# Kernel optimization log

Hardware: AMD Instinct MI355X
Metric: run time of the kernel (lower is better)

## Reference

```python
import jax, jax.numpy as jnp
import numpy as np

N_TAYLOR = 4

def taylor_exp_poly(x, n_terms):
    # sum_{p=0}^{n_terms-1} x^p / p!  via Horner: 1 + x*(1 + x/2*(1 + x/3*(...)))
    acc = jnp.ones_like(x)
    for p in range(n_terms - 1, 0, -1):
        acc = 1.0 + (x / p) * acc
    return acc

def setup_inputs() -> dict:
    key = jax.random.key(0)
    kq, kk, kv = jax.random.split(key, 3)
    B, H, T, d_key, d_val = 4, 8, 2048, 32, 64
    Q = jax.random.normal(kq, (B, H, T, d_key), dtype=jnp.float32)
    K = jax.random.normal(kk, (B, H, T, d_key), dtype=jnp.float32)
    V = jax.random.normal(kv, (B, H, T, d_val), dtype=jnp.float32)
    return {"Q": Q, "K": K, "V": V}

def reference(Q, K, V):
    # Symmetry-aware Taylor-approximated attention (Heinsen & Kozachkov).
    # The tightly-packed degree-p feature maps phi_p satisfy
    #   phi_p(q) . phi_p(k) == (q.k / sqrt(d_key))^p / p!
    # so summing S/Z over all n_taylor terms equals attention with kernel
    #   w(q,k) = sum_{p<n_taylor} (q.k/sqrt(d_key))^p / p!   (truncated exp),
    # causally masked and normalized by the row-sum Z.
    d_key = Q.shape[-1]
    scale = 1.0 / jnp.sqrt(jnp.asarray(d_key, dtype=Q.dtype))
    scores = jnp.einsum('bhqd,bhkd->bhqk', Q, K) * scale  # [B,H,T,T]
    A = taylor_exp_poly(scores, N_TAYLOR)
    T = Q.shape[-2]
    causal = jnp.tril(jnp.ones((T, T), dtype=bool))  # [T,T]
    A = jnp.where(causal, A, jnp.zeros((), dtype=A.dtype))
    Z = jnp.sum(A, axis=-1, keepdims=True)           # [B,H,T,1]
    S = jnp.einsum('bhqk,bhkd->bhqd', A, V)          # [B,H,T,d_val]
    return S / Z
```

## Files before the change

kernel.cpp:

```cpp
#include <hip/hip_runtime.h>
#include <hip/hip_bf16.h>


typedef __attribute__((ext_vector_type(8))) short bf16x8;
typedef __attribute__((ext_vector_type(8))) _Float16 f16x8;
typedef __attribute__((ext_vector_type(4))) float f32x4;
typedef __attribute__((ext_vector_type(16))) float f32x16;
typedef unsigned int u32;
typedef unsigned short u16;

namespace {

constexpr int T_SEQ = 2048;
constexpr int DK    = 32;
constexpr int DV    = 64;
constexpr int NBH   = 32;

constexpr float C1 = 0.17677669529663687f;
constexpr float C2 = 0.015625f;
constexpr float C3 = 9.2071195e-4f;

constexpr size_t KHF_OFF  = 0;
constexpr size_t VTHI_OFF = (size_t)NBH * T_SEQ * DK * 2;
constexpr size_t WS_NEED  = VTHI_OFF + (size_t)NBH * DV * T_SEQ * 2;

__device__ __forceinline__ u32 pack_hi2(float f0, float f1) {
  return (__float_as_uint(f0) >> 16) | (__float_as_uint(f1) & 0xffff0000u);
}
__device__ __forceinline__ float trunc_bf(float f) {
  return __uint_as_float(__float_as_uint(f) & 0xffff0000u);
}
__device__ __forceinline__ u16 f2h(float f) {
  union { _Float16 h; u16 u; } c;
  c.h = (_Float16)f;
  return c.u;
}
__device__ __forceinline__ u32 pack_rn2(float f0, float f1) {
  union { __hip_bfloat16 h; u16 u; } a, b;
  a.h = __hip_bfloat16(f0);
  b.h = __hip_bfloat16(f1);
  return (u32)a.u | ((u32)b.u << 16);
}
__device__ __forceinline__ void permswap(u32& a, u32& b) {
  asm volatile("v_permlane32_swap_b32 %0, %1" : "+v"(a), "+v"(b));
}


__global__ void pack_kv(const float* __restrict__ Kg, const float* __restrict__ Vg,
                        u16* __restrict__ Khf, u16* __restrict__ Vthi) {
  __shared__ float tile[DV][33];
  const int bid = blockIdx.x;
  const int t   = threadIdx.x;
  if (bid < 2048) {
    size_t i = ((size_t)bid * 256 + t) * 4;
    float4 f = *(const float4*)(Kg + i);
    ushort4 h;
    h.x = f2h(f.x); h.y = f2h(f.y); h.z = f2h(f.z); h.w = f2h(f.w);
    *(ushort4*)(Khf + i) = h;
  } else {
    const int vb = bid - 2048;
    const int bh = vb >> 6;
    const int k0 = (vb & 63) * 32;
    {
      const int kl = t >> 3, c0 = (t & 7) * 8;
      const float* src = Vg + ((size_t)bh * T_SEQ + k0 + kl) * DV + c0;
      float4 a = *(const float4*)src;
      float4 b = *(const float4*)(src + 4);
      tile[c0 + 0][kl] = a.x; tile[c0 + 1][kl] = a.y;
      tile[c0 + 2][kl] = a.z; tile[c0 + 3][kl] = a.w;
      tile[c0 + 4][kl] = b.x; tile[c0 + 5][kl] = b.y;
      tile[c0 + 6][kl] = b.z; tile[c0 + 7][kl] = b.w;
    }
    __syncthreads();
    {
      const int cl = t >> 2, k8 = (t & 3) * 8;
      u32 h[4];
#pragma unroll
      for (int j = 0; j < 4; ++j)
        h[j] = pack_rn2(tile[cl][k8 + 2 * j], tile[cl][k8 + 2 * j + 1]);
      size_t off = ((size_t)(bh * DV + cl)) * T_SEQ + k0 + k8;
      *(uint4*)(Vthi + off) = make_uint4(h[0], h[1], h[2], h[3]);
    }
  }
}


__global__ __launch_bounds__(256, 4)
void taylor_attn_v7(const float* __restrict__ Qg, const u16* __restrict__ Khf,
                    const u16* __restrict__ Vthi, float* __restrict__ Outg) {
  __shared__ __align__(16) float Sp[4 * 2048];
  __shared__ float Zp[4 * 32];

  const int tid = threadIdx.x;
  const int l   = tid & 63;
  const int w   = tid >> 6;
  const int cq  = l & 31;
  const int hi  = l >> 5;

  const int bid = blockIdx.x;
  const int xcd = bid & 7;
  const int r_  = bid >> 3;
  const int bh  = xcd * 4 + (r_ & 3);
  const int p   = r_ >> 2;

  const u16* kq = Khf + (size_t)bh * T_SEQ * DK + (size_t)cq * DK + hi * 8;
  const u16* vq = Vthi + (size_t)bh * DV * T_SEQ + (size_t)cq * T_SEQ + hi * 8;
  const float* qb = Qg + (size_t)bh * T_SEQ * DK;

#pragma unroll 1
  for (int ph = 0; ph < 2; ++ph) {
    const int s  = ph ? (63 - p) : p;
    const int q0 = s * 32;

    if (ph) __syncthreads();

    f16x8 qf[2];
#pragma unroll
    for (int t = 0; t < 2; ++t) {
      const float* qp = qb + (size_t)(q0 + cq) * DK + t * 16 + hi * 8;
      float4 a = *(const float4*)qp;
      float4 b = *(const float4*)(qp + 4);
      f16x8 v;
      v[0] = (_Float16)a.x; v[1] = (_Float16)a.y;
      v[2] = (_Float16)a.z; v[3] = (_Float16)a.w;
      v[4] = (_Float16)b.x; v[5] = (_Float16)b.y;
      v[6] = (_Float16)b.z; v[7] = (_Float16)b.w;
      qf[t] = v;
    }

    f32x16 acc0, acc1;
#pragma unroll
    for (int r = 0; r < 16; ++r) { acc0[r] = 0.f; acc1[r] = 0.f; }
    float zacc = 0.f;

    auto LOADK = [&](f16x8* kf, int kt) {
      const u16* kp = kq + (size_t)kt * 1024;
      kf[0] = *(const f16x8*)kp;
      kf[1] = *(const f16x8*)(kp + 16);
    };
    auto LOADV = [&](bf16x8* vf, int kt) {
#pragma unroll
      for (int ct = 0; ct < 2; ++ct)
#pragma unroll
        for (int t = 0; t < 2; ++t)
          vf[ct * 2 + t] = *(const bf16x8*)(
              vq + (size_t)ct * 32 * T_SEQ + kt * 32 + t * 16);
    };
    auto STEP = [&](const f16x8* kf, const bf16x8* vf, bool diag) {
      f32x16 d;
#pragma unroll
      for (int r = 0; r < 16; ++r) d[r] = 0.f;
      d = __builtin_amdgcn_mfma_f32_32x32x16_f16(kf[0], qf[0], d, 0, 0, 0);
      d = __builtin_amdgcn_mfma_f32_32x32x16_f16(kf[1], qf[1], d, 0, 0, 0);
      float wv[16];
#pragma unroll
      for (int r = 0; r < 16; ++r) {
        float sc = d[r];
        float t_ = __builtin_fmaf(sc, C3, C2);
        t_       = __builtin_fmaf(sc, t_, C1);
        float wr = __builtin_fmaf(sc, t_, 1.0f);
        if (diag) {
          const int krel = (r & 3) + 8 * (r >> 2) + 4 * hi;
          wr = (krel <= cq) ? wr : 0.f;
        }
        zacc += wr;
        wv[r] = wr;
      }
      union { bf16x8 v; u32 u[4]; } WH[2];
#pragma unroll
      for (int t = 0; t < 2; ++t) {
        const int b = t * 8;
        u32 p0 = pack_rn2(wv[b + 0], wv[b + 1]);
        u32 p1 = pack_rn2(wv[b + 2], wv[b + 3]);
        u32 p2 = pack_rn2(wv[b + 4], wv[b + 5]);
        u32 p3 = pack_rn2(wv[b + 6], wv[b + 7]);
        permswap(p0, p2); permswap(p1, p3);
        WH[t].u[0] = p0; WH[t].u[1] = p1; WH[t].u[2] = p2; WH[t].u[3] = p3;
      }
      acc0 = __builtin_amdgcn_mfma_f32_32x32x16_bf16(WH[0].v, vf[0], acc0, 0, 0, 0);
      acc0 = __builtin_amdgcn_mfma_f32_32x32x16_bf16(WH[1].v, vf[1], acc0, 0, 0, 0);
      acc1 = __builtin_amdgcn_mfma_f32_32x32x16_bf16(WH[0].v, vf[2], acc1, 0, 0, 0);
      acc1 = __builtin_amdgcn_mfma_f32_32x32x16_bf16(WH[1].v, vf[3], acc1, 0, 0, 0);
    };

    int kt = w;
    f16x8 kA[2], kB[2];
    if (kt < s) {
      LOADK(kA, kt);
      while (true) {
        int kn = kt + 4;
        if (kn < s) {
          LOADK(kB, kn);
          bf16x8 vf[4]; LOADV(vf, kt);
          STEP(kA, vf, false);
          kt = kn;
        } else {
          bf16x8 vf[4]; LOADV(vf, kt);
          STEP(kA, vf, false);
          break;
        }
        kn = kt + 4;
        if (kn < s) {
          LOADK(kA, kn);
          bf16x8 vf[4]; LOADV(vf, kt);
          STEP(kB, vf, false);
          kt = kn;
        } else {
          bf16x8 vf[4]; LOADV(vf, kt);
          STEP(kB, vf, false);
          break;
        }
      }
    }
    if ((s & 3) == w) {
      f16x8 kD[2]; LOADK(kD, s);
      bf16x8 vf[4]; LOADV(vf, s);
      STEP(kD, vf, true);
    }

    {
      float zt = zacc + __shfl_xor(zacc, 32);
      if (hi == 0) Zp[w * 32 + cq] = zt;
    }
#pragma unroll
    for (int r = 0; r < 16; ++r) {
      const int qr = (r & 3) + 8 * (r >> 2) + 4 * hi;
      Sp[w * 2048 + qr * 64 + cq]      = acc0[r];
      Sp[w * 2048 + qr * 64 + 32 + cq] = acc1[r];
    }
    __syncthreads();

    const f32x4* S4 = (const f32x4*)Sp;
#pragma unroll
    for (int i = 0; i < 2; ++i) {
      const int e4  = tid + i * 256;
      const int row = e4 >> 4;
      f32x4 ssum = S4[e4] + S4[512 + e4] + S4[1024 + e4] + S4[1536 + e4];
      float z = Zp[row] + Zp[32 + row] + Zp[64 + row] + Zp[96 + row];
      float inv = 1.0f / z;
      float4 o;
      o.x = ssum[0] * inv; o.y = ssum[1] * inv;
      o.z = ssum[2] * inv; o.w = ssum[3] * inv;
      *(float4*)(Outg + ((size_t)bh * T_SEQ + q0 + row) * DV + (e4 & 15) * 4) = o;
    }
  }
}


constexpr int QT_FB = 64;
constexpr int KT_FB = 32;
constexpr int LDSW  = 40;
constexpr float SCALE = 0.17677669529663687f;

__global__ __launch_bounds__(256, 4)
void taylor_attn_fb(const float* __restrict__ Qg, const float* __restrict__ Kg,
                    const float* __restrict__ Vg, float* __restrict__ Outg) {
  __shared__ __align__(16) unsigned short Qhi[QT_FB * LDSW], Qlo[QT_FB * LDSW];
  __shared__ __align__(16) unsigned short Khi_[KT_FB * LDSW], Klo_[KT_FB * LDSW];
  __shared__ __align__(16) unsigned short Vthi_[DV * LDSW], Vtlo_[DV * LDSW];
  __shared__ __align__(16) unsigned Wp[4][16 * 32];

  const int tid  = threadIdx.x;
  const int lane = tid & 63;
  const int wid  = tid >> 6;
  const int m    = lane & 15;
  const int g    = lane >> 4;

  const int bid = blockIdx.x;
  const int v   = bid >> 3;
  const int bh  = (bid & 7) * 4 + (v >> 5);
  const int qt  = 31 - (v & 31);
  const int q0  = qt * QT_FB;

  const float* Qbase = Qg + ((size_t)bh * T_SEQ + q0) * DK;
  const float* Kbase = Kg + (size_t)bh * T_SEQ * DK;
  const float* Vbase = Vg + (size_t)bh * T_SEQ * DV;

#pragma unroll
  for (int p = 0; p < 2; ++p) {
    int e = tid + p * 256, row = e >> 3, c4 = (e & 7) * 4;
    float4 f = *(const float4*)(Qbase + row * DK + c4);
    uint2 h, l;
    h.x = pack_hi2(f.x, f.y); h.y = pack_hi2(f.z, f.w);
    l.x = pack_hi2(f.x - trunc_bf(f.x), f.y - trunc_bf(f.y));
    l.y = pack_hi2(f.z - trunc_bf(f.z), f.w - trunc_bf(f.w));
    *(uint2*)&Qhi[row * LDSW + c4] = h;
    *(uint2*)&Qlo[row * LDSW + c4] = l;
  }
  __syncthreads();

  const int wq = wid * 16;
  const bf16x8 qhi = *(const bf16x8*)&Qhi[(wq + m) * LDSW + g * 8];
  const bf16x8 qlo = *(const bf16x8*)&Qlo[(wq + m) * LDSW + g * 8];

  f32x4 acc[4];
#pragma unroll
  for (int ct = 0; ct < 4; ++ct) acc[ct] = f32x4{0.f, 0.f, 0.f, 0.f};
  float zacc[4] = {0.f, 0.f, 0.f, 0.f};

  const int q_lane0 = q0 + wq + g * 4;
  const int q_wave_max = q0 + wq + 15;

  const int nkt = (q0 + QT_FB) / KT_FB;
  for (int kt = 0; kt < nkt; ++kt) {
    const int k0 = kt * KT_FB;
    __syncthreads();
    {
      int row = tid >> 3, c4 = (tid & 7) * 4;
      float4 f = *(const float4*)(Kbase + (size_t)(k0 + row) * DK + c4);
      uint2 h, l;
      h.x = pack_hi2(f.x, f.y); h.y = pack_hi2(f.z, f.w);
      l.x = pack_hi2(f.x - trunc_bf(f.x), f.y - trunc_bf(f.y));
      l.y = pack_hi2(f.z - trunc_bf(f.z), f.w - trunc_bf(f.w));
      *(uint2*)&Khi_[row * LDSW + c4] = h;
      *(uint2*)&Klo_[row * LDSW + c4] = l;
    }
    {
      int kk = (tid & 15) * 2, c4 = (tid >> 4) * 4;
      const float* vp = Vbase + (size_t)(k0 + kk) * DV + c4;
      float4 a = *(const float4*)vp;
      float4 b = *(const float4*)(vp + DV);
      float af[4] = {a.x, a.y, a.z, a.w};
      float bf_[4] = {b.x, b.y, b.z, b.w};
#pragma unroll
      for (int jj = 0; jj < 4; ++jj) {
        *(unsigned*)&Vthi_[(c4 + jj) * LDSW + kk] = pack_hi2(af[jj], bf_[jj]);
        *(unsigned*)&Vtlo_[(c4 + jj) * LDSW + kk] =
            pack_hi2(af[jj] - trunc_bf(af[jj]), bf_[jj] - trunc_bf(bf_[jj]));
      }
    }
    __syncthreads();

    if (k0 > q_wave_max) continue;

#pragma unroll
    for (int k16 = 0; k16 < 2; ++k16) {
      const int kcol0 = k16 * 16;
      bf16x8 khi = *(const bf16x8*)&Khi_[(kcol0 + m) * LDSW + g * 8];
      bf16x8 klo = *(const bf16x8*)&Klo_[(kcol0 + m) * LDSW + g * 8];
      f32x4 sc = {0.f, 0.f, 0.f, 0.f};
      sc = __builtin_amdgcn_mfma_f32_16x16x32_bf16(qhi, khi, sc, 0, 0, 0);
      sc = __builtin_amdgcn_mfma_f32_16x16x32_bf16(qhi, klo, sc, 0, 0, 0);
      sc = __builtin_amdgcn_mfma_f32_16x16x32_bf16(qlo, khi, sc, 0, 0, 0);
      const int k_abs = k0 + kcol0 + m;
      const int kcol  = kcol0 + m;
#pragma unroll
      for (int r = 0; r < 4; ++r) {
        float x  = sc[r] * SCALE;
        float a3 = __builtin_fmaf(x, 0.3333333333333333f, 1.0f);
        float a2 = __builtin_fmaf(x * 0.5f, a3, 1.0f);
        float wvv = __builtin_fmaf(x, a2, 1.0f);
        wvv = (k_abs <= q_lane0 + r) ? wvv : 0.0f;
        zacc[r] += wvv;
        float wl = wvv - trunc_bf(wvv);
        unsigned packed = (__float_as_uint(wvv) >> 16) |
                          (__float_as_uint(wl) & 0xffff0000u);
        const int q = g * 4 + r;
        Wp[wid][q * 32 + (((kcol >> 2) ^ (q & 7)) << 2) + (kcol & 3)] = packed;
      }
    }

    uint4 pa = *(const uint4*)&Wp[wid][m * 32 + (((2 * g) ^ (m & 7)) << 2)];
    uint4 pb = *(const uint4*)&Wp[wid][m * 32 + (((2 * g + 1) ^ (m & 7)) << 2)];
    union { bf16x8 v; unsigned u[4]; } WH, WL;
    WH.u[0] = (pa.x & 0xffffu) | (pa.y << 16);
    WH.u[1] = (pa.z & 0xffffu) | (pa.w << 16);
    WH.u[2] = (pb.x & 0xffffu) | (pb.y << 16);
    WH.u[3] = (pb.z & 0xffffu) | (pb.w << 16);
    WL.u[0] = (pa.x >> 16) | (pa.y & 0xffff0000u);
    WL.u[1] = (pa.z >> 16) | (pa.w & 0xffff0000u);
    WL.u[2] = (pb.x >> 16) | (pb.y & 0xffff0000u);
    WL.u[3] = (pb.z >> 16) | (pb.w & 0xffff0000u);

#pragma unroll
    for (int ct = 0; ct < 4; ++ct) {
      bf16x8 vhi = *(const bf16x8*)&Vthi_[(ct * 16 + m) * LDSW + g * 8];
      bf16x8 vlo = *(const bf16x8*)&Vtlo_[(ct * 16 + m) * LDSW + g * 8];
      acc[ct] = __builtin_amdgcn_mfma_f32_16x16x32_bf16(WH.v, vhi, acc[ct], 0, 0, 0);
      acc[ct] = __builtin_amdgcn_mfma_f32_16x16x32_bf16(WH.v, vlo, acc[ct], 0, 0, 0);
      acc[ct] = __builtin_amdgcn_mfma_f32_16x16x32_bf16(WL.v, vhi, acc[ct], 0, 0, 0);
    }
  }

  float invz[4];
#pragma unroll
  for (int r = 0; r < 4; ++r) {
    float z = zacc[r];
    z += __shfl_xor(z, 1); z += __shfl_xor(z, 2);
    z += __shfl_xor(z, 4); z += __shfl_xor(z, 8);
    invz[r] = 1.0f / z;
  }

  float* ob = Outg + ((size_t)bh * T_SEQ + (q0 + wq)) * DV;
#pragma unroll
  for (int ct = 0; ct < 4; ++ct)
#pragma unroll
    for (int r = 0; r < 4; ++r)
      ob[(g * 4 + r) * DV + ct * 16 + m] = acc[ct][r] * invz[r];
}

}

extern "C" void kernel_launch(void* const* d_in, const int* in_sizes, int n_in,
                              void* d_out, int out_size, void* d_ws, size_t ws_size,
                              hipStream_t stream) {
  const float* Q = (const float*)d_in[0];
  const float* K = (const float*)d_in[1];
  const float* V = (const float*)d_in[2];
  float* Out = (float*)d_out;

  if (ws_size >= WS_NEED && d_ws != nullptr) {
    u16* khf  = (u16*)((char*)d_ws + KHF_OFF);
    u16* vthi = (u16*)((char*)d_ws + VTHI_OFF);

    hipLaunchKernelGGL(pack_kv, dim3(4096), dim3(256), 0, stream, K, V, khf, vthi);
    hipLaunchKernelGGL(taylor_attn_v7, dim3(1024), dim3(256), 0, stream,
                       Q, khf, vthi, Out);
  } else {
    hipLaunchKernelGGL(taylor_attn_fb, dim3(1024), dim3(256), 0, stream,
                       Q, K, V, Out);
  }
}
```

Measured before the change: 55.69 us.

## Process four query tiles per block with software-pipelined QK and double-buffered LDS

After: 56.85 us. 1.02x slower.

```diff
diff --git a/kernel.cpp b/kernel.cpp
--- a/kernel.cpp
+++ b/kernel.cpp
@@ -85,11 +85,11 @@
 }
 
 
-__global__ __launch_bounds__(256, 4)
-void taylor_attn_v7(const float* __restrict__ Qg, const u16* __restrict__ Khf,
+__global__ __launch_bounds__(256, 2)
+void taylor_attn_v8(const float* __restrict__ Qg, const u16* __restrict__ Khf,
                     const u16* __restrict__ Vthi, float* __restrict__ Outg) {
-  __shared__ __align__(16) float Sp[4 * 2048];
-  __shared__ float Zp[4 * 32];
+  __shared__ __align__(16) float Sp[2][4 * 2048];
+  __shared__ float Zp[2][4 * 32];
 
   const int tid = threadIdx.x;
   const int l   = tid & 63;
@@ -101,18 +101,23 @@
   const int xcd = bid & 7;
   const int r_  = bid >> 3;
   const int bh  = xcd * 4 + (r_ & 3);
-  const int p   = r_ >> 2;
+  const int pp  = r_ >> 2;
 
   const u16* kq = Khf + (size_t)bh * T_SEQ * DK + (size_t)cq * DK + hi * 8;
   const u16* vq = Vthi + (size_t)bh * DV * T_SEQ + (size_t)cq * T_SEQ + hi * 8;
   const float* qb = Qg + (size_t)bh * T_SEQ * DK;
 
+  f32x16 ZERO;
+#pragma unroll
+  for (int r = 0; r < 16; ++r) ZERO[r] = 0.f;
+
 #pragma unroll 1
-  for (int ph = 0; ph < 2; ++ph) {
-    const int s  = ph ? (63 - p) : p;
+  for (int ph = 0; ph < 4; ++ph) {
+    const int s  = (ph == 0) ? pp : (ph == 1) ? (63 - pp)
+                 : (ph == 2) ? (16 + pp) : (47 - pp);
     const int q0 = s * 32;
-
-    if (ph) __syncthreads();
+    float* SpH = &Sp[ph & 1][0];
+    float* ZpH = &Zp[ph & 1][0];
 
     f16x8 qf[2];
 #pragma unroll
@@ -128,10 +133,8 @@
       qf[t] = v;
     }
 
-    f32x16 acc0, acc1;
-#pragma unroll
-    for (int r = 0; r < 16; ++r) { acc0[r] = 0.f; acc1[r] = 0.f; }
-    float zacc = 0.f;
+    f32x16 acc0 = ZERO, acc1 = ZERO;
+    float zpa = 0.f, zpb = 0.f, zpc = 0.f, zpd = 0.f;
 
     auto LOADK = [&](f16x8* kf, int kt) {
       const u16* kp = kq + (size_t)kt * 1024;
@@ -146,12 +149,11 @@
           vf[ct * 2 + t] = *(const bf16x8*)(
               vq + (size_t)ct * 32 * T_SEQ + kt * 32 + t * 16);
     };
-    auto STEP = [&](const f16x8* kf, const bf16x8* vf, bool diag) {
-      f32x16 d;
-#pragma unroll
-      for (int r = 0; r < 16; ++r) d[r] = 0.f;
-      d = __builtin_amdgcn_mfma_f32_32x32x16_f16(kf[0], qf[0], d, 0, 0, 0);
-      d = __builtin_amdgcn_mfma_f32_32x32x16_f16(kf[1], qf[1], d, 0, 0, 0);
+    auto QK = [&](const f16x8* kf) -> f32x16 {
+      f32x16 d = __builtin_amdgcn_mfma_f32_32x32x16_f16(kf[0], qf[0], ZERO, 0, 0, 0);
+      return __builtin_amdgcn_mfma_f32_32x32x16_f16(kf[1], qf[1], d, 0, 0, 0);
+    };
+    auto FINISH = [&](const f32x16& d, const bf16x8* vf, bool diag) {
       float wv[16];
 #pragma unroll
       for (int r = 0; r < 16; ++r) {
@@ -163,9 +165,12 @@
           const int krel = (r & 3) + 8 * (r >> 2) + 4 * hi;
           wr = (krel <= cq) ? wr : 0.f;
         }
-        zacc += wr;
         wv[r] = wr;
       }
+      zpa += (wv[0] + wv[4]) + (wv[8]  + wv[12]);
+      zpb += (wv[1] + wv[5]) + (wv[9]  + wv[13]);
+      zpc += (wv[2] + wv[6]) + (wv[10] + wv[14]);
+      zpd += (wv[3] + wv[7]) + (wv[11] + wv[15]);
       union { bf16x8 v; u32 u[4]; } WH[2];
 #pragma unroll
       for (int t = 0; t < 2; ++t) {
@@ -183,60 +188,61 @@
       acc1 = __builtin_amdgcn_mfma_f32_32x32x16_bf16(WH[1].v, vf[3], acc1, 0, 0, 0);
     };
 
-    int kt = w;
-    f16x8 kA[2], kB[2];
-    if (kt < s) {
-      LOADK(kA, kt);
-      while (true) {
+    {
+      int kt = w;
+      if (kt < s) {
+        f16x8 kA[2], kB[2];
+        bf16x8 vA[4], vB[4];
+        f32x16 dA, dB;
+        LOADK(kA, kt);
+        LOADV(vA, kt);
         int kn = kt + 4;
-        if (kn < s) {
-          LOADK(kB, kn);
-          bf16x8 vf[4]; LOADV(vf, kt);
-          STEP(kA, vf, false);
-          kt = kn;
-        } else {
-          bf16x8 vf[4]; LOADV(vf, kt);
-          STEP(kA, vf, false);
-          break;
-        }
-        kn = kt + 4;
-        if (kn < s) {
-          LOADK(kA, kn);
-          bf16x8 vf[4]; LOADV(vf, kt);
-          STEP(kB, vf, false);
-          kt = kn;
-        } else {
-          bf16x8 vf[4]; LOADV(vf, kt);
-          STEP(kB, vf, false);
-          break;
+        bool haveB = (kn < s);
+        if (haveB) { LOADK(kB, kn); LOADV(vB, kn); }
+        dA = QK(kA);
+        while (true) {
+          if (!haveB) { FINISH(dA, vA, false); break; }
+          dB = QK(kB);
+          { int k2 = kn + 4; if (k2 < s) LOADK(kA, k2); }
+          FINISH(dA, vA, false);
+          { int k2 = kn + 4; if (k2 < s) LOADV(vA, k2); }
+          kt = kn; kn = kt + 4; haveB = (kn < s);
+          if (!haveB) { FINISH(dB, vB, false); break; }
+          dA = QK(kA);
+          { int k2 = kn + 4; if (k2 < s) LOADK(kB, k2); }
+          FINISH(dB, vB, false);
+          { int k2 = kn + 4; if (k2 < s) LOADV(vB, k2); }
+          kt = kn; kn = kt + 4; haveB = (kn < s);
         }
       }
     }
     if ((s & 3) == w) {
       f16x8 kD[2]; LOADK(kD, s);
-      bf16x8 vf[4]; LOADV(vf, s);
-      STEP(kD, vf, true);
-    }
-
-    {
+      bf16x8 vD[4]; LOADV(vD, s);
+      f32x16 dD = QK(kD);
+      FINISH(dD, vD, true);
+    }
+
+    {
+      float zacc = (zpa + zpb) + (zpc + zpd);
       float zt = zacc + __shfl_xor(zacc, 32);
-      if (hi == 0) Zp[w * 32 + cq] = zt;
+      if (hi == 0) ZpH[w * 32 + cq] = zt;
     }
 #pragma unroll
     for (int r = 0; r < 16; ++r) {
       const int qr = (r & 3) + 8 * (r >> 2) + 4 * hi;
-      Sp[w * 2048 + qr * 64 + cq]      = acc0[r];
-      Sp[w * 2048 + qr * 64 + 32 + cq] = acc1[r];
+      SpH[w * 2048 + qr * 64 + cq]      = acc0[r];
+      SpH[w * 2048 + qr * 64 + 32 + cq] = acc1[r];
     }
     __syncthreads();
 
-    const f32x4* S4 = (const f32x4*)Sp;
+    const f32x4* S4 = (const f32x4*)SpH;
 #pragma unroll
     for (int i = 0; i < 2; ++i) {
       const int e4  = tid + i * 256;
       const int row = e4 >> 4;
       f32x4 ssum = S4[e4] + S4[512 + e4] + S4[1024 + e4] + S4[1536 + e4];
-      float z = Zp[row] + Zp[32 + row] + Zp[64 + row] + Zp[96 + row];
+      float z = ZpH[row] + ZpH[32 + row] + ZpH[64 + row] + ZpH[96 + row];
       float inv = 1.0f / z;
       float4 o;
       o.x = ssum[0] * inv; o.y = ssum[1] * inv;
@@ -414,7 +420,7 @@
     u16* vthi = (u16*)((char*)d_ws + VTHI_OFF);
 
     hipLaunchKernelGGL(pack_kv, dim3(4096), dim3(256), 0, stream, K, V, khf, vthi);
-    hipLaunchKernelGGL(taylor_attn_v7, dim3(1024), dim3(256), 0, stream,
+    hipLaunchKernelGGL(taylor_attn_v8, dim3(512), dim3(256), 0, stream,
                        Q, khf, vthi, Out);
   } else {
     hipLaunchKernelGGL(taylor_attn_fb, dim3(1024), dim3(256), 0, stream,
```
